# Kernel tuning notes

Hardware: AMD Instinct MI355X
Metric: run time of the kernel (lower is better)

## Reference

```python
import jax, jax.numpy as jnp
import numpy as np

EPS = 1e-5


def _rln(x, w, b, m1w, m1b, m2w, m2b):
    # Revised LayerNorm (DehazeFormer): per-sample stats over (C,H,W)
    mean = jnp.mean(x, axis=(1, 2, 3), keepdims=True)            # [b,1,1,1]
    std = jnp.sqrt(jnp.mean((x - mean) ** 2, axis=(1, 2, 3), keepdims=True) + EPS)
    normed = (x - mean) / std * w + b                            # [b,C,H,W]
    rescale = std * m1w + m1b                                    # 1x1 conv from 1 channel
    rebias = mean * m2w + m2b
    return normed, rescale, rebias


def _pconv(x, W, b):
    # 1x1 conv as channel contraction: W [out,in], x [b,in,h,w]
    return jnp.einsum('oi,bihw->bohw', W, x) + b[None, :, None, None]


def setup_inputs() -> dict:
    key = jax.random.key(0)
    ks = jax.random.split(key, 24)
    B, C, H, W = 8, 96, 128, 128
    p = lambda k, shp, s=0.02: (jax.random.normal(k, shp, dtype=jnp.float32) * s)
    inp = {
        'x_u': jax.random.normal(ks[0], (B, C, H, W), dtype=jnp.float32),
        'x_d': jax.random.normal(ks[1], (B, C, H, W), dtype=jnp.float32),
        # RLN (u)
        'nw_u': jnp.ones((1, C, 1, 1), jnp.float32),
        'nb_u': jnp.zeros((1, C, 1, 1), jnp.float32),
        'm1w_u': p(ks[2], (1, C, 1, 1)), 'm1b_u': p(ks[3], (1, C, 1, 1)),
        'm2w_u': p(ks[4], (1, C, 1, 1)), 'm2b_u': p(ks[5], (1, C, 1, 1)),
        # RLN (d)
        'nw_d': jnp.ones((1, C, 1, 1), jnp.float32),
        'nb_d': jnp.zeros((1, C, 1, 1), jnp.float32),
        'm1w_d': p(ks[6], (1, C, 1, 1)), 'm1b_d': p(ks[7], (1, C, 1, 1)),
        'm2w_d': p(ks[8], (1, C, 1, 1)), 'm2b_d': p(ks[9], (1, C, 1, 1)),
        # 1x1 qkv convs
        'Wqkv_u': p(ks[10], (2 * C, C)), 'bqkv_u': jnp.zeros((2 * C,), jnp.float32),
        'Wqkv_d': p(ks[11], (2 * C, C)), 'bqkv_d': jnp.zeros((2 * C,), jnp.float32),
        # learned scalar scales
        'scale_h': jnp.ones((1,), jnp.float32),
        'scale_w': jnp.ones((1,), jnp.float32),
        'scale_c': jnp.ones((1,), jnp.float32),
    }
    return inp


def reference(x_u, x_d,
              nw_u, nb_u, m1w_u, m1b_u, m2w_u, m2b_u,
              nw_d, nb_d, m1w_d, m1b_d, m2w_d, m2b_d,
              Wqkv_u, bqkv_u, Wqkv_d, bqkv_d,
              scale_h, scale_w, scale_c):
    x_d_norm, resc_d, bias_d = _rln(x_d, nw_d, nb_d, m1w_d, m1b_d, m2w_d, m2b_d)
    x_u_norm, resc_u, bias_u = _rln(x_u, nw_u, nb_u, m1w_u, m1b_u, m2w_u, m2b_u)

    q_u, v_u = jnp.split(_pconv(x_u_norm, Wqkv_u, bqkv_u), 2, axis=1)
    k_d, v_d = jnp.split(_pconv(x_d_norm, Wqkv_d, bqkv_d), 2, axis=1)

    q_h, q_w, q_c = jnp.split(q_u, 3, axis=1)
    k_h, k_w, k_c = jnp.split(k_d, 3, axis=1)
    vu_h, vu_w, vu_c = jnp.split(v_u, 3, axis=1)
    vd_h, vd_w, vd_c = jnp.split(v_d, 3, axis=1)

    # ---- height-axis attention: per (b,w), scores over h x h ----
    A_h = jax.nn.softmax(jnp.einsum('bciw,bcjw->bwij', q_h, k_h) * scale_h[0], axis=-1)
    d2u_h = jnp.einsum('bwij,bcjw->bciw', A_h, vd_h)            # attn @ v_d
    u2d_h = jnp.einsum('bwij,bciw->bcjw', A_h, vu_h)            # attn^T @ v_u

    # ---- width-axis attention: per (b,h), scores over w x w ----
    S_w = jnp.einsum('bchi,bchj->bhij', q_w, k_w) * scale_w[0]
    d2u_w = jnp.einsum('bhij,bchj->bchi', jax.nn.softmax(S_w, axis=-1), vd_w)
    # softmax(S_w^T, -1) @ v_u  ==  softmax over axis -2, contracted over i
    u2d_w = jnp.einsum('bhij,bchi->bchj', jax.nn.softmax(S_w, axis=-2), vu_w)

    # ---- channel-axis attention: per b, scores over c x c ----
    b, c, h, w = q_c.shape
    qc = q_c.reshape(b, c, h * w)
    kc = k_c.reshape(b, c, h * w)
    A_c = jax.nn.softmax(jnp.einsum('bcn,bdn->bcd', qc, kc) * scale_c[0], axis=-1)
    d2u_c = jnp.einsum('bcd,bdn->bcn', A_c, vd_c.reshape(b, c, h * w)).reshape(b, c, h, w)
    # NOTE: original code uses the same (non-transposed) softmax for u2d_c
    u2d_c = jnp.einsum('bcd,bdn->bcn', A_c, vu_c.reshape(b, c, h * w)).reshape(b, c, h, w)

    x_d2u = jnp.concatenate([d2u_h, d2u_w, d2u_c], axis=1)
    x_u2d = jnp.concatenate([u2d_h, u2d_w, u2d_c], axis=1)

    out_u = x_d2u * resc_u + bias_u + x_u
    out_d = x_u2d * resc_d + bias_d + x_d
    return out_u + out_d
```

## Files before the change

### kernel.cpp

```cpp
#include <hip/hip_runtime.h>
#include <math.h>

#define NB 8
#define NC 96
#define NH 128
#define NWID 128
#define NN (NH*NWID)
#define NCO 192
#define NM (NC*NN)

#define WS_SUMS   0
#define WS_SC     32
#define WS_AC     8224
#define WS_SU     16416
#define WS_TU     17184
#define WS_SD     17952
#define WS_TD     18720
#define WS_RU     19488
#define WS_RD     20256
#define WS_CADD   21024
#define WS_BPU    21792
#define WS_BPD    23328
#define WS_WB16   24864
#define WS_QKV16  327680
#define QKV16_D   25165824ull
#define WS_SLABS  25493504
#define OFF_QH    0ull
#define OFF_KH    5242880ull
#define OFF_QW    10485760ull
#define OFF_KW    15728640ull
#define OFF_VHU   20971520ull
#define OFF_VHD   25427968ull
#define OFF_VWU   29884416ull
#define OFF_VWD   34340864ull
#define WS_OH     44892160

typedef __attribute__((ext_vector_type(8))) short bf16x8;
typedef __attribute__((ext_vector_type(4))) float f32x4;

static __device__ __forceinline__ float bf2f(ushort u){ return __uint_as_float(((uint)u) << 16); }
static __device__ __forceinline__ ushort f2bf(float f){
  uint b = __float_as_uint(f);
  return (ushort)((b + 0x7fffu + ((b >> 16) & 1u)) >> 16);
}
static __device__ __forceinline__ bf16x8 ldfrag(const ushort* p){
  union { uint4 u; bf16x8 b; } cv; cv.u = *(const uint4*)p; return cv.b;
}

__global__ __launch_bounds__(256) void reduce_stats(const float* __restrict__ xu,
                                                    const float* __restrict__ xd,
                                                    float* __restrict__ ws) {
  int blk = blockIdx.x;
  int tensor = blk >> 9;
  int b = (blk >> 6) & 7;
  int chunk = blk & 63;
  const float* x = tensor ? xd : xu;
  const float4* p = (const float4*)(x + (size_t)b*NM + (size_t)chunk*(NM/64));
  float s = 0.f, sq = 0.f;
  for (int r = 0; r < 24; r++) {
    float4 v = p[threadIdx.x + r*256];
    s  += v.x + v.y + v.z + v.w;
    sq += v.x*v.x + v.y*v.y + v.z*v.z + v.w*v.w;
  }
  for (int o = 32; o; o >>= 1) { s += __shfl_down(s, o); sq += __shfl_down(sq, o); }
  __shared__ float ls[8];
  int wv = threadIdx.x >> 6, ln = threadIdx.x & 63;
  if (ln == 0) { ls[wv*2] = s; ls[wv*2+1] = sq; }
  __syncthreads();
  if (threadIdx.x == 0) {
    s  = ls[0] + ls[2] + ls[4] + ls[6];
    sq = ls[1] + ls[3] + ls[5] + ls[7];
    atomicAdd(&ws[WS_SUMS + (tensor*8 + b)*2],     s);
    atomicAdd(&ws[WS_SUMS + (tensor*8 + b)*2 + 1], sq);
  }
}

__global__ void compute_params(float* __restrict__ ws,
    const float* __restrict__ nwu, const float* __restrict__ nbu,
    const float* __restrict__ m1wu, const float* __restrict__ m1bu,
    const float* __restrict__ m2wu, const float* __restrict__ m2bu,
    const float* __restrict__ nwd, const float* __restrict__ nbd,
    const float* __restrict__ m1wd, const float* __restrict__ m1bd,
    const float* __restrict__ m2wd, const float* __restrict__ m2bd,
    const float* __restrict__ Wqu, const float* __restrict__ bqu,
    const float* __restrict__ Wqd, const float* __restrict__ bqd) {
  __shared__ float meanL[16], stdL[16];
  __shared__ float tuL[768], tdL[768];
  int t = threadIdx.x;
  if (t < 16) {
    float s = ws[WS_SUMS + t*2], sq = ws[WS_SUMS + t*2 + 1];
    const float inv = 1.f / (float)NM;
    float mean = s * inv;
    float var  = sq * inv - mean*mean;
    meanL[t] = mean;
    stdL[t]  = sqrtf(var + 1e-5f);
  }
  __syncthreads();
  for (int idx = t; idx < 768; idx += 256) {
    int b = idx / 96, c = idx % 96;
    float mu = meanL[b],   su = stdL[b];
    float md = meanL[8+b], sd = stdL[8+b];
    float scu = nwu[c] / su;
    float scd = nwd[c] / sd;
    float tcu = nbu[c] - mu*scu;
    float tcd = nbd[c] - md*scd;
    tuL[idx] = tcu; tdL[idx] = tcd;
    ws[WS_SU+idx] = scu; ws[WS_TU+idx] = tcu;
    ws[WS_SD+idx] = scd; ws[WS_TD+idx] = tcd;
    ws[WS_RU+idx] = su*m1wu[c] + m1bu[c];
    ws[WS_RD+idx] = sd*m1wd[c] + m1bd[c];
    ws[WS_CADD+idx] = (mu*m2wu[c] + m2bu[c]) + (md*m2wd[c] + m2bd[c]);
  }
  __syncthreads();
  for (int idx = t; idx < 3072; idx += 256) {
    int tensor = idx / 1536;
    int r = idx % 1536;
    int b = r / 192, o = r % 192;
    const float* Wq = tensor ? Wqd : Wqu;
    const float* tt = tensor ? tdL : tuL;
    float acc = tensor ? bqd[o] : bqu[o];
    for (int i = 0; i < 96; i++) acc += Wq[o*96 + i] * tt[b*96 + i];
    ws[(tensor ? WS_BPD : WS_BPU) + r] = acc;
  }
}

__global__ __launch_bounds__(256) void compute_wprime(float* __restrict__ ws,
    const float* __restrict__ Wqu, const float* __restrict__ Wqd) {
  int idx = blockIdx.x*256 + threadIdx.x;
  if (idx >= 319488) return;
  int tensor = idx / 159744;
  int r = idx % 159744;
  int b  = r / 19968;
  int r2 = r % 19968;
  int o  = r2 / 104, i = r2 % 104;
  ushort* wb = (ushort*)(ws + WS_WB16);
  ushort v = 0;
  if (i < 96) {
    const float* Wq = tensor ? Wqd : Wqu;
    const float* s  = ws + (tensor ? WS_SD : WS_SU);
    v = f2bf(Wq[o*96 + i] * s[b*96 + i]);
  }
  wb[idx] = v;
}

__global__ __launch_bounds__(256) void qkv_gemm(float* __restrict__ ws,
    const float* __restrict__ xu, const float* __restrict__ xd) {
  __shared__ __align__(16) ushort QL[33280];
  ushort* Al = QL;
  ushort* Bl = QL + 19968;
  int blk = blockIdx.x;
  int tensor = blk >> 10;
  int rem = blk & 1023;
  int b = rem >> 7;
  int nt = rem & 127;
  int n0 = nt*128;
  const float* x = (tensor ? xd : xu) + (size_t)b*NM;
  const ushort* wb = (const ushort*)(ws + WS_WB16) + (size_t)(tensor*8 + b)*19968;
  const float* bp = ws + (tensor ? WS_BPD : WS_BPU) + b*192;
  ushort* outq16 = (ushort*)(ws + WS_QKV16) + (tensor ? QKV16_D : 0) + (size_t)b*NCO*NN;
  ushort* slab = (ushort*)(ws + WS_SLABS);
  const int t = threadIdx.x;
  const int wv = t >> 6, lid = t & 63, l15 = lid & 15, l4 = lid >> 4;

  for (int it = 0; it < 10; it++) {
    int idx = t + it*256;
    if (idx < 2496) ((uint4*)Al)[idx] = ((const uint4*)wb)[idx];
  }
  for (int it = 0; it < 6; it++) {
    int idx = t + it*256;
    int i2 = (idx & 7) | ((idx >> 8) << 3);
    int n4 = (idx >> 3) & 31;
    const float* r0 = x + (size_t)(2*i2)*NN + n0 + n4*4;
    float4 a0 = *(const float4*)r0;
    float4 a1 = *(const float4*)(r0 + NN);
    uint p0 = (uint)f2bf(a0.x) | ((uint)f2bf(a1.x) << 16);
    uint p1 = (uint)f2bf(a0.y) | ((uint)f2bf(a1.y) << 16);
    uint p2 = (uint)f2bf(a0.z) | ((uint)f2bf(a1.z) << 16);
    uint p3 = (uint)f2bf(a0.w) | ((uint)f2bf(a1.w) << 16);
    ushort* base = &Bl[(size_t)(n4*4)*104 + 2*i2];
    *(uint*)(base)           = p0;
    *(uint*)(base + 104)     = p1;
    *(uint*)(base + 208)     = p2;
    *(uint*)(base + 312)     = p3;
  }
  __syncthreads();

  f32x4 z4 = {0.f,0.f,0.f,0.f};
  f32x4 acc[12][2];
  #pragma unroll
  for (int mt = 0; mt < 12; mt++) { acc[mt][0] = z4; acc[mt][1] = z4; }
  #pragma unroll
  for (int s = 0; s < 3; s++) {
    bf16x8 b0 = ldfrag(&Bl[((2*wv+0)*16 + l15)*104 + s*32 + l4*8]);
    bf16x8 b1 = ldfrag(&Bl[((2*wv+1)*16 + l15)*104 + s*32 + l4*8]);
    #pragma unroll
    for (int mt = 0; mt < 12; mt++) {
      bf16x8 a = ldfrag(&Al[(mt*16 + l15)*104 + s*32 + l4*8]);
      acc[mt][0] = __builtin_amdgcn_mfma_f32_16x16x32_bf16(a, b0, acc[mt][0], 0, 0, 0);
      acc[mt][1] = __builtin_amdgcn_mfma_f32_16x16x32_bf16(a, b1, acc[mt][1], 0, 0, 0);
    }
  }
  __syncthreads();
  ushort* Cl = QL;
  #pragma unroll
  for (int mt = 0; mt < 12; mt++) {
    #pragma unroll
    for (int r = 0; r < 4; r++) {
      int o = mt*16 + l4*4 + r;
      float bb = bp[o];
      Cl[o*128 + 32*wv + l15]      = f2bf(acc[mt][0][r] + bb);
      Cl[o*128 + 32*wv + 16 + l15] = f2bf(acc[mt][1][r] + bb);
    }
  }
  __syncthreads();
  for (int it = 0; it < 6; it++) {
    int idx = t + it*256;
    int lr = idx >> 4, ch = idx & 15;
    int o = (lr < 64) ? (64 + lr) : (96 + lr);
    *(uint4*)(outq16 + (size_t)o*NN + n0 + ch*8) = *(const uint4*)&Cl[o*128 + ch*8];
  }
  {
    int axis = t >> 7, w = t & 127;
    ushort* dstq = slab + (tensor ? (axis ? OFF_KW : OFF_KH) : (axis ? OFF_QW : OFF_QH));
    size_t o = axis ? ((size_t)(b*128 + nt)*128 + w)*40
                    : ((size_t)(b*128 + w)*128 + nt)*40;
    uint uu[16];
    #pragma unroll
    for (int k = 0; k < 16; k++) {
      ushort a0 = Cl[(axis*32 + 2*k)*128 + w];
      ushort a1 = Cl[(axis*32 + 2*k + 1)*128 + w];
      uu[k] = (uint)a0 | ((uint)a1 << 16);
    }
    *(uint4*)(dstq + o)      = make_uint4(uu[0],uu[1],uu[2],uu[3]);
    *(uint4*)(dstq + o + 8)  = make_uint4(uu[4],uu[5],uu[6],uu[7]);
    *(uint4*)(dstq + o + 16) = make_uint4(uu[8],uu[9],uu[10],uu[11]);
    *(uint4*)(dstq + o + 24) = make_uint4(uu[12],uu[13],uu[14],uu[15]);
  }
  {
    ushort* dstv = slab + (tensor ? OFF_VWD : OFF_VWU);
    for (int k = 0; k < 2; k++) {
      int idx = t + k*256;
      int c = idx >> 4, ch = idx & 15;
      *(uint4*)(dstv + ((size_t)(b*128 + nt)*32 + c)*136 + ch*8) =
          *(const uint4*)&Cl[(128 + c)*128 + ch*8];
    }
  }
}

__global__ __launch_bounds__(256) void qkv_prep(float* __restrict__ ws) {
  __shared__ __align__(16) ushort Br[16*1320];
  int bid = blockIdx.x;
  int tensor = bid >> 8;
  int r = bid & 255;
  int cb = r >> 7, b = (r >> 4) & 7, hb = (r >> 2) & 3, wb = r & 3;
  const ushort* qkv16 = (const ushort*)(ws + WS_QKV16);
  const ushort* src = qkv16 + (tensor ? QKV16_D : 0)
                    + (size_t)b*NCO*NN + (size_t)(96 + cb*16)*NN;
  ushort* dst = (ushort*)(ws + WS_SLABS) + (tensor ? OFF_VHD : OFF_VHU);
  int t = threadIdx.x;
  for (int k = 0; k < 8; k++) {
    int idx = t + k*256;
    int c = idx >> 7, h = (idx >> 2) & 31, w8 = idx & 3;
    uint4 v = *(const uint4*)(src + (size_t)c*NN + (size_t)(hb*32 + h)*NWID + wb*32 + w8*8);
    *(uint4*)&Br[c*1320 + h*40 + w8*8] = v;
  }
  __syncthreads();
  for (int k = 0; k < 2; k++) {
    int idx = t + k*256;
    int w = idx >> 4, c = idx & 15;
    uint uu[16];
    #pragma unroll
    for (int hh = 0; hh < 16; hh++) {
      ushort a0 = Br[c*1320 + (2*hh)*40 + w];
      ushort a1 = Br[c*1320 + (2*hh+1)*40 + w];
      uu[hh] = (uint)a0 | ((uint)a1 << 16);
    }
    size_t o = ((size_t)(b*128 + wb*32 + w)*32 + cb*16 + c)*136 + hb*32;
    *(uint4*)(dst + o)      = make_uint4(uu[0],uu[1],uu[2],uu[3]);
    *(uint4*)(dst + o + 8)  = make_uint4(uu[4],uu[5],uu[6],uu[7]);
    *(uint4*)(dst + o + 16) = make_uint4(uu[8],uu[9],uu[10],uu[11]);
    *(uint4*)(dst + o + 24) = make_uint4(uu[12],uu[13],uu[14],uu[15]);
  }
}

template<int AXIS>
__global__ __launch_bounds__(256) void attn_mfma(float* __restrict__ ws,
    const float* __restrict__ xu, const float* __restrict__ xd,
    float* __restrict__ out, const float* __restrict__ scale_p) {
  __shared__ __align__(16) ushort Qs[128*40];
  __shared__ __align__(16) ushort Ks[128*40];
  __shared__ __align__(16) ushort Vds[32*136];
  __shared__ __align__(16) ushort Vus[32*136];
  __shared__ __align__(16) ushort Pl[128*136];
  __shared__ float m1s[128], l1s[128];
  const int b = blockIdx.x >> 7, p2 = blockIdx.x & 127;
  const int t = threadIdx.x;
  const int wv = t >> 6, lid = t & 63, l15 = lid & 15, l4 = lid >> 4;
  const ushort* slab = (const ushort*)(ws + WS_SLABS);
  const ushort* qsrc  = slab + (AXIS ? OFF_QW : OFF_QH) + (size_t)(b*128 + p2)*5120;
  const ushort* ksrc  = slab + (AXIS ? OFF_KW : OFF_KH) + (size_t)(b*128 + p2)*5120;
  const ushort* vdsrc = slab + (AXIS ? OFF_VWD : OFF_VHD) + (size_t)(b*128 + p2)*4352;
  const ushort* vusrc = slab + (AXIS ? OFF_VWU : OFF_VHU) + (size_t)(b*128 + p2)*4352;
  for (int i = t; i < 2368; i += 256) {
    const uint4* s; uint4* d;
    if (i < 640)       { s = (const uint4*)qsrc + i;          d = (uint4*)Qs + i; }
    else if (i < 1280) { s = (const uint4*)ksrc + (i-640);    d = (uint4*)Ks + (i-640); }
    else if (i < 1824) { s = (const uint4*)vdsrc + (i-1280);  d = (uint4*)Vds + (i-1280); }
    else               { s = (const uint4*)vusrc + (i-1824);  d = (uint4*)Vus + (i-1824); }
    *d = *s;
  }
  const float sc = scale_p[0];
  const int cbas = AXIS ? 32 : 0;
  float ruv0 = ws[WS_RU + b*96 + cbas + l15];
  float ruv1 = ws[WS_RU + b*96 + cbas + 16 + l15];
  float rdv0 = ws[WS_RD + b*96 + cbas + l15];
  float rdv1 = ws[WS_RD + b*96 + cbas + 16 + l15];
  __syncthreads();

  f32x4 z4 = {0.f,0.f,0.f,0.f};
  f32x4 s1[2][8];
  {
    bf16x8 bfr[8];
    #pragma unroll
    for (int tj = 0; tj < 8; tj++) bfr[tj] = ldfrag(&Ks[(tj*16 + l15)*40 + l4*8]);
    #pragma unroll
    for (int ti = 0; ti < 2; ti++) {
      bf16x8 a = ldfrag(&Qs[((2*wv+ti)*16 + l15)*40 + l4*8]);
      #pragma unroll
      for (int tj = 0; tj < 8; tj++)
        s1[ti][tj] = __builtin_amdgcn_mfma_f32_16x16x32_bf16(a, bfr[tj], z4, 0, 0, 0);
    }
  }
  #pragma unroll
  for (int ti = 0; ti < 2; ti++) {
    #pragma unroll
    for (int r = 0; r < 4; r++) {
      float mx = -3.0e38f;
      #pragma unroll
      for (int tj = 0; tj < 8; tj++) { float v = s1[ti][tj][r]*sc; s1[ti][tj][r] = v; mx = fmaxf(mx, v); }
      mx = fmaxf(mx, __shfl_xor(mx, 1)); mx = fmaxf(mx, __shfl_xor(mx, 2));
      mx = fmaxf(mx, __shfl_xor(mx, 4)); mx = fmaxf(mx, __shfl_xor(mx, 8));
      float sm = 0.f;
      #pragma unroll
      for (int tj = 0; tj < 8; tj++) { float e = __expf(s1[ti][tj][r] - mx); s1[ti][tj][r] = e; sm += e; }
      sm += __shfl_xor(sm, 1); sm += __shfl_xor(sm, 2); sm += __shfl_xor(sm, 4); sm += __shfl_xor(sm, 8);
      int row = 32*wv + ti*16 + l4*4 + r;
      if (l15 == 0) { m1s[row] = mx; l1s[row] = sm; }
      float inv = __fdividef(1.f, sm);
      #pragma unroll
      for (int tj = 0; tj < 8; tj++) Pl[row*136 + tj*16 + l15] = f2bf(s1[ti][tj][r]*inv);
    }
  }
  __syncthreads();
  f32x4 o1[2][2] = {{z4,z4},{z4,z4}};
  #pragma unroll
  for (int ks = 0; ks < 4; ks++) {
    bf16x8 bv0 = ldfrag(&Vds[l15*136 + ks*32 + l4*8]);
    bf16x8 bv1 = ldfrag(&Vds[(16 + l15)*136 + ks*32 + l4*8]);
    #pragma unroll
    for (int mt = 0; mt < 2; mt++) {
      bf16x8 a = ldfrag(&Pl[((2*wv+mt)*16 + l15)*136 + ks*32 + l4*8]);
      o1[mt][0] = __builtin_amdgcn_mfma_f32_16x16x32_bf16(a, bv0, o1[mt][0], 0, 0, 0);
      o1[mt][1] = __builtin_amdgcn_mfma_f32_16x16x32_bf16(a, bv1, o1[mt][1], 0, 0, 0);
    }
  }
  {
    bf16x8 bq[8];
    #pragma unroll
    for (int it = 0; it < 8; it++) bq[it] = ldfrag(&Qs[(it*16 + l15)*40 + l4*8]);
    #pragma unroll
    for (int tjt = 0; tjt < 2; tjt++) {
      bf16x8 a = ldfrag(&Ks[((2*wv+tjt)*16 + l15)*40 + l4*8]);
      #pragma unroll
      for (int it = 0; it < 8; it++)
        s1[tjt][it] = __builtin_amdgcn_mfma_f32_16x16x32_bf16(a, bq[it], z4, 0, 0, 0);
    }
  }
  if (AXIS == 1) {
    #pragma unroll
    for (int tjt = 0; tjt < 2; tjt++) {
      #pragma unroll
      for (int r = 0; r < 4; r++) {
        float mx = -3.0e38f;
        #pragma unroll
        for (int it = 0; it < 8; it++) { float v = s1[tjt][it][r]*sc; s1[tjt][it][r] = v; mx = fmaxf(mx, v); }
        mx = fmaxf(mx, __shfl_xor(mx, 1)); mx = fmaxf(mx, __shfl_xor(mx, 2));
        mx = fmaxf(mx, __shfl_xor(mx, 4)); mx = fmaxf(mx, __shfl_xor(mx, 8));
        float sm = 0.f;
        #pragma unroll
        for (int it = 0; it < 8; it++) { float e = __expf(s1[tjt][it][r] - mx); s1[tjt][it][r] = e; sm += e; }
        sm += __shfl_xor(sm, 1); sm += __shfl_xor(sm, 2); sm += __shfl_xor(sm, 4); sm += __shfl_xor(sm, 8);
        float inv = __fdividef(1.f, sm);
        #pragma unroll
        for (int it = 0; it < 8; it++) s1[tjt][it][r] *= inv;
      }
    }
  } else {
    float mi[8], li[8];
    #pragma unroll
    for (int it = 0; it < 8; it++) {
      mi[it] = m1s[it*16 + l15];
      li[it] = __fdividef(1.f, l1s[it*16 + l15]);
    }
    #pragma unroll
    for (int tjt = 0; tjt < 2; tjt++)
      #pragma unroll
      for (int it = 0; it < 8; it++)
        #pragma unroll
        for (int r = 0; r < 4; r++)
          s1[tjt][it][r] = __expf(s1[tjt][it][r]*sc - mi[it]) * li[it];
  }
  __syncthreads();
  #pragma unroll
  for (int tjt = 0; tjt < 2; tjt++)
    #pragma unroll
    for (int r = 0; r < 4; r++) {
      int row = 32*wv + tjt*16 + l4*4 + r;
      #pragma unroll
      for (int it = 0; it < 8; it++) Pl[row*136 + it*16 + l15] = f2bf(s1[tjt][it][r]);
    }
  __syncthreads();
  f32x4 o2[2][2] = {{z4,z4},{z4,z4}};
  #pragma unroll
  for (int ks = 0; ks < 4; ks++) {
    bf16x8 bv0 = ldfrag(&Vus[l15*136 + ks*32 + l4*8]);
    bf16x8 bv1 = ldfrag(&Vus[(16 + l15)*136 + ks*32 + l4*8]);
    #pragma unroll
    for (int mt = 0; mt < 2; mt++) {
      bf16x8 a = ldfrag(&Pl[((2*wv+mt)*16 + l15)*136 + ks*32 + l4*8]);
      o2[mt][0] = __builtin_amdgcn_mfma_f32_16x16x32_bf16(a, bv0, o2[mt][0], 0, 0, 0);
      o2[mt][1] = __builtin_amdgcn_mfma_f32_16x16x32_bf16(a, bv1, o2[mt][1], 0, 0, 0);
    }
  }
  __syncthreads();
  float* St = (float*)Pl;
  #pragma unroll
  for (int mt = 0; mt < 2; mt++)
    #pragma unroll
    for (int nt = 0; nt < 2; nt++) {
      float ru = nt ? ruv1 : ruv0;
      float rd = nt ? rdv1 : rdv0;
      float4 vv;
      vv.x = o1[mt][nt][0]*ru + o2[mt][nt][0]*rd;
      vv.y = o1[mt][nt][1]*ru + o2[mt][nt][1]*rd;
      vv.z = o1[mt][nt][2]*ru + o2[mt][nt][2]*rd;
      vv.w = o1[mt][nt][3]*ru + o2[mt][nt][3]*rd;
      *(float4*)&St[(nt*16 + l15)*132 + (2*wv+mt)*16 + l4*4] = vv;
    }
  __syncthreads();
  if (AXIS == 1) {
    for (int k = 0; k < 4; k++) {
      int idx = t + k*256;
      int c = idx >> 5, p4 = idx & 31;
      float4 v = *(const float4*)&St[c*132 + p4*4];
      float ca = ws[WS_CADD + b*96 + 32 + c];
      size_t off = ((size_t)(b*NC + 32 + c)*NH + p2)*NWID + p4*4;
      float4 a = *(const float4*)(xu + off);
      float4 dd = *(const float4*)(xd + off);
      v.x += ca + a.x + dd.x; v.y += ca + a.y + dd.y;
      v.z += ca + a.z + dd.z; v.w += ca + a.w + dd.w;
      *(float4*)(out + off) = v;
    }
  } else {
    float* oh = ws + WS_OH;
    for (int k = 0; k < 4; k++) {
      int idx = t + k*256;
      int c = idx >> 5, p4 = idx & 31;
      float4 v = *(const float4*)&St[c*132 + p4*4];
      *(float4*)(oh + ((size_t)(b*128 + p2)*32 + c)*128 + p4*4) = v;
    }
  }
}

__global__ __launch_bounds__(256) void merge_h(float* __restrict__ ws,
    const float* __restrict__ xu, const float* __restrict__ xd,
    float* __restrict__ out) {
  __shared__ float T[32][33];
  int bid = blockIdx.x;
  int b = bid >> 9, c = (bid >> 4) & 31, ht = (bid >> 2) & 3, wt = bid & 3;
  int t = threadIdx.x;
  const float* oh = ws + WS_OH;
  {
    int w = t >> 3, h4 = t & 7;
    float4 v = *(const float4*)(oh + ((size_t)(b*128 + wt*32 + w)*32 + c)*128 + ht*32 + h4*4);
    T[w][h4*4+0] = v.x; T[w][h4*4+1] = v.y; T[w][h4*4+2] = v.z; T[w][h4*4+3] = v.w;
  }
  __syncthreads();
  {
    int h = t >> 3, w4 = t & 7;
    float ca = ws[WS_CADD + b*96 + c];
    size_t off = ((size_t)(b*NC + c)*NH + ht*32 + h)*NWID + wt*32 + w4*4;
    float4 a = *(const float4*)(xu + off);
    float4 d = *(const float4*)(xd + off);
    float4 v;
    v.x = T[w4*4+0][h] + ca + a.x + d.x;
    v.y = T[w4*4+1][h] + ca + a.y + d.y;
    v.z = T[w4*4+2][h] + ca + a.z + d.z;
    v.w = T[w4*4+3][h] + ca + a.w + d.w;
    *(float4*)(out + off) = v;
  }
}

__global__ __launch_bounds__(256) void attn_c1(float* __restrict__ ws) {
  __shared__ float qs[32][260], ks[32][260];
  int b = blockIdx.x >> 6, chunk = blockIdx.x & 63;
  int n0 = chunk * 256;
  int t = threadIdx.x;
  const ushort* qkv16 = (const ushort*)(ws + WS_QKV16);
  const ushort* qp = qkv16 + ((size_t)b*NCO + 64)*NN + n0;
  const ushort* kp = qkv16 + QKV16_D + ((size_t)b*NCO + 64)*NN + n0;
  for (int r = 0; r < 4; r++) {
    int idx = t + r*256;
    int c = idx >> 5, n8 = idx & 31;
    uint4 v = *(const uint4*)(qp + (size_t)c*NN + n8*8);
    uint4 w = *(const uint4*)(kp + (size_t)c*NN + n8*8);
    float* q = &qs[c][n8*8];
    float* kk = &ks[c][n8*8];
    q[0] = bf2f((ushort)(v.x & 0xffff)); q[1] = bf2f((ushort)(v.x >> 16));
    q[2] = bf2f((ushort)(v.y & 0xffff)); q[3] = bf2f((ushort)(v.y >> 16));
    q[4] = bf2f((ushort)(v.z & 0xffff)); q[5] = bf2f((ushort)(v.z >> 16));
    q[6] = bf2f((ushort)(v.w & 0xffff)); q[7] = bf2f((ushort)(v.w >> 16));
    kk[0] = bf2f((ushort)(w.x & 0xffff)); kk[1] = bf2f((ushort)(w.x >> 16));
    kk[2] = bf2f((ushort)(w.y & 0xffff)); kk[3] = bf2f((ushort)(w.y >> 16));
    kk[4] = bf2f((ushort)(w.z & 0xffff)); kk[5] = bf2f((ushort)(w.z >> 16));
    kk[6] = bf2f((ushort)(w.w & 0xffff)); kk[7] = bf2f((ushort)(w.w >> 16));
  }
  __syncthreads();
  int d = t & 31, cbq = t >> 5;
  float a[4] = {0.f,0.f,0.f,0.f};
  for (int n4 = 0; n4 < 64; n4++) {
    float4 kv = *(const float4*)&ks[d][n4*4];
    #pragma unroll
    for (int r = 0; r < 4; r++) {
      float4 qv = *(const float4*)&qs[cbq + 8*r][n4*4];
      a[r] += qv.x*kv.x + qv.y*kv.y + qv.z*kv.z + qv.w*kv.w;
    }
  }
  #pragma unroll
  for (int r = 0; r < 4; r++)
    atomicAdd(&ws[WS_SC + b*1024 + (cbq + 8*r)*32 + d], a[r]);
}

__global__ void attn_c2(float* __restrict__ ws, const float* __restrict__ scale_p) {
  int b = blockIdx.x, c = threadIdx.x;
  if (c >= 32) return;
  float sc = scale_p[0];
  float row[32];
  float m = -3.0e38f;
  for (int d = 0; d < 32; d++) { row[d] = ws[WS_SC + b*1024 + c*32 + d] * sc; m = fmaxf(m, row[d]); }
  float s = 0.f;
  for (int d = 0; d < 32; d++) { row[d] = __expf(row[d] - m); s += row[d]; }
  float inv = 1.f / s;
  for (int d = 0; d < 32; d++) ws[WS_AC + b*1024 + c*32 + d] = row[d]*inv;
}

__global__ __launch_bounds__(256) void attn_c3(float* __restrict__ ws,
    const float* __restrict__ xu, const float* __restrict__ xd,
    float* __restrict__ out) {
  __shared__ float AsT[32][36];
  __shared__ float ruL[32], rdL[32], caL[32];
  int b = blockIdx.x >> 6, chunk = blockIdx.x & 63;
  int t = threadIdx.x;
  for (int r = 0; r < 4; r++) {
    int idx = t + r*256;
    int c = idx >> 5, d = idx & 31;
    AsT[d][c] = ws[WS_AC + b*1024 + idx];
  }
  if (t < 32) {
    ruL[t] = ws[WS_RU + b*96 + 64 + t];
    rdL[t] = ws[WS_RD + b*96 + 64 + t];
    caL[t] = ws[WS_CADD + b*96 + 64 + t];
  }
  __syncthreads();
  int n = chunk*256 + t;
  const ushort* qkv16 = (const ushort*)(ws + WS_QKV16);
  const ushort* vdp = qkv16 + QKV16_D + ((size_t)b*NCO + 160)*NN + n;
  const ushort* vup = qkv16 + ((size_t)b*NCO + 160)*NN + n;
  float acc1[32], acc2[32];
  #pragma unroll
  for (int c2 = 0; c2 < 32; c2++) { acc1[c2]=0.f; acc2[c2]=0.f; }
  for (int d = 0; d < 32; d++) {
    float vd = bf2f(vdp[(size_t)d*NN]);
    float vu = bf2f(vup[(size_t)d*NN]);
    #pragma unroll
    for (int c4 = 0; c4 < 8; c4++) {
      float4 av = *(const float4*)&AsT[d][c4*4];
      acc1[c4*4+0] += av.x*vd; acc2[c4*4+0] += av.x*vu;
      acc1[c4*4+1] += av.y*vd; acc2[c4*4+1] += av.y*vu;
      acc1[c4*4+2] += av.z*vd; acc2[c4*4+2] += av.z*vu;
      acc1[c4*4+3] += av.w*vd; acc2[c4*4+3] += av.w*vu;
    }
  }
  size_t base = ((size_t)(b*NC) + 64)*NN + n;
  #pragma unroll
  for (int c2 = 0; c2 < 32; c2++) {
    size_t off = base + (size_t)c2*NN;
    out[off] = acc1[c2]*ruL[c2] + acc2[c2]*rdL[c2] + caL[c2] + xu[off] + xd[off];
  }
}

extern "C" void kernel_launch(void* const* d_in, const int* in_sizes, int n_in,
                              void* d_out, int out_size, void* d_ws, size_t ws_size,
                              hipStream_t stream) {
  (void)in_sizes; (void)n_in; (void)out_size; (void)ws_size;
  const float* xu   = (const float*)d_in[0];
  const float* xd   = (const float*)d_in[1];
  const float* nwu  = (const float*)d_in[2];
  const float* nbu  = (const float*)d_in[3];
  const float* m1wu = (const float*)d_in[4];
  const float* m1bu = (const float*)d_in[5];
  const float* m2wu = (const float*)d_in[6];
  const float* m2bu = (const float*)d_in[7];
  const float* nwd  = (const float*)d_in[8];
  const float* nbd  = (const float*)d_in[9];
  const float* m1wd = (const float*)d_in[10];
  const float* m1bd = (const float*)d_in[11];
  const float* m2wd = (const float*)d_in[12];
  const float* m2bd = (const float*)d_in[13];
  const float* Wqu  = (const float*)d_in[14];
  const float* bqu  = (const float*)d_in[15];
  const float* Wqd  = (const float*)d_in[16];
  const float* bqd  = (const float*)d_in[17];
  const float* sch  = (const float*)d_in[18];
  const float* scw  = (const float*)d_in[19];
  const float* scc  = (const float*)d_in[20];
  float* ws  = (float*)d_ws;
  float* out = (float*)d_out;

  hipMemsetAsync(d_ws, 0, 8224*sizeof(float), stream);
  reduce_stats<<<1024, 256, 0, stream>>>(xu, xd, ws);
  compute_params<<<1, 256, 0, stream>>>(ws, nwu, nbu, m1wu, m1bu, m2wu, m2bu,
                                        nwd, nbd, m1wd, m1bd, m2wd, m2bd,
                                        Wqu, bqu, Wqd, bqd);
  compute_wprime<<<1248, 256, 0, stream>>>(ws, Wqu, Wqd);
  qkv_gemm<<<2048, 256, 0, stream>>>(ws, xu, xd);
  qkv_prep<<<512, 256, 0, stream>>>(ws);
  attn_mfma<0><<<1024, 256, 0, stream>>>(ws, xu, xd, out, sch);
  attn_mfma<1><<<1024, 256, 0, stream>>>(ws, xu, xd, out, scw);
  merge_h<<<4096, 256, 0, stream>>>(ws, xu, xd, out);
  attn_c1<<<512, 256, 0, stream>>>(ws);
  attn_c2<<<8, 64, 0, stream>>>(ws, scc);
  attn_c3<<<512, 256, 0, stream>>>(ws, xu, xd, out);
}
```

Measured before the change: 256.7 us.

## Read QKV weights directly from global, pad output tile, store H-attention output as bf16

```diff
diff --git a/kernel.cpp b/kernel.cpp
--- a/kernel.cpp
+++ b/kernel.cpp
@@ -145,9 +145,8 @@
 
 __global__ __launch_bounds__(256) void qkv_gemm(float* __restrict__ ws,
     const float* __restrict__ xu, const float* __restrict__ xd) {
-  __shared__ __align__(16) ushort QL[33280];
-  ushort* Al = QL;
-  ushort* Bl = QL + 19968;
+  __shared__ __align__(16) ushort QL[26112];
+  ushort* Bl = QL;
   int blk = blockIdx.x;
   int tensor = blk >> 10;
   int rem = blk & 1023;
@@ -162,10 +161,6 @@
   const int t = threadIdx.x;
   const int wv = t >> 6, lid = t & 63, l15 = lid & 15, l4 = lid >> 4;
 
-  for (int it = 0; it < 10; it++) {
-    int idx = t + it*256;
-    if (idx < 2496) ((uint4*)Al)[idx] = ((const uint4*)wb)[idx];
-  }
   for (int it = 0; it < 6; it++) {
     int idx = t + it*256;
     int i2 = (idx & 7) | ((idx >> 8) << 3);
@@ -195,7 +190,7 @@
     bf16x8 b1 = ldfrag(&Bl[((2*wv+1)*16 + l15)*104 + s*32 + l4*8]);
     #pragma unroll
     for (int mt = 0; mt < 12; mt++) {
-      bf16x8 a = ldfrag(&Al[(mt*16 + l15)*104 + s*32 + l4*8]);
+      bf16x8 a = ldfrag(&wb[(mt*16 + l15)*104 + s*32 + l4*8]);
       acc[mt][0] = __builtin_amdgcn_mfma_f32_16x16x32_bf16(a, b0, acc[mt][0], 0, 0, 0);
       acc[mt][1] = __builtin_amdgcn_mfma_f32_16x16x32_bf16(a, b1, acc[mt][1], 0, 0, 0);
     }
@@ -208,8 +203,8 @@
     for (int r = 0; r < 4; r++) {
       int o = mt*16 + l4*4 + r;
       float bb = bp[o];
-      Cl[o*128 + 32*wv + l15]      = f2bf(acc[mt][0][r] + bb);
-      Cl[o*128 + 32*wv + 16 + l15] = f2bf(acc[mt][1][r] + bb);
+      Cl[o*136 + 32*wv + l15]      = f2bf(acc[mt][0][r] + bb);
+      Cl[o*136 + 32*wv + 16 + l15] = f2bf(acc[mt][1][r] + bb);
     }
   }
   __syncthreads();
@@ -217,7 +212,7 @@
     int idx = t + it*256;
     int lr = idx >> 4, ch = idx & 15;
     int o = (lr < 64) ? (64 + lr) : (96 + lr);
-    *(uint4*)(outq16 + (size_t)o*NN + n0 + ch*8) = *(const uint4*)&Cl[o*128 + ch*8];
+    *(uint4*)(outq16 + (size_t)o*NN + n0 + ch*8) = *(const uint4*)&Cl[o*136 + ch*8];
   }
   {
     int axis = t >> 7, w = t & 127;
@@ -227,8 +222,8 @@
     uint uu[16];
     #pragma unroll
     for (int k = 0; k < 16; k++) {
-      ushort a0 = Cl[(axis*32 + 2*k)*128 + w];
-      ushort a1 = Cl[(axis*32 + 2*k + 1)*128 + w];
+      ushort a0 = Cl[(axis*32 + 2*k)*136 + w];
+      ushort a1 = Cl[(axis*32 + 2*k + 1)*136 + w];
       uu[k] = (uint)a0 | ((uint)a1 << 16);
     }
     *(uint4*)(dstq + o)      = make_uint4(uu[0],uu[1],uu[2],uu[3]);
@@ -242,7 +237,7 @@
       int idx = t + k*256;
       int c = idx >> 4, ch = idx & 15;
       *(uint4*)(dstv + ((size_t)(b*128 + nt)*32 + c)*136 + ch*8) =
-          *(const uint4*)&Cl[(128 + c)*128 + ch*8];
+          *(const uint4*)&Cl[(128 + c)*136 + ch*8];
     }
   }
 }
@@ -462,12 +457,17 @@
       *(float4*)(out + off) = v;
     }
   } else {
-    float* oh = ws + WS_OH;
-    for (int k = 0; k < 4; k++) {
+    ushort* oh16 = (ushort*)(ws + WS_OH);
+    for (int k = 0; k < 2; k++) {
       int idx = t + k*256;
-      int c = idx >> 5, p4 = idx & 31;
-      float4 v = *(const float4*)&St[c*132 + p4*4];
-      *(float4*)(oh + ((size_t)(b*128 + p2)*32 + c)*128 + p4*4) = v;
+      int c = idx >> 4, p8 = idx & 15;
+      const float* src = &St[c*132 + p8*8];
+      uint4 pk;
+      pk.x = (uint)f2bf(src[0]) | ((uint)f2bf(src[1]) << 16);
+      pk.y = (uint)f2bf(src[2]) | ((uint)f2bf(src[3]) << 16);
+      pk.z = (uint)f2bf(src[4]) | ((uint)f2bf(src[5]) << 16);
+      pk.w = (uint)f2bf(src[6]) | ((uint)f2bf(src[7]) << 16);
+      *(uint4*)(oh16 + ((size_t)(b*128 + p2)*32 + c)*128 + p8*8) = pk;
     }
   }
 }
@@ -479,11 +479,14 @@
   int bid = blockIdx.x;
   int b = bid >> 9, c = (bid >> 4) & 31, ht = (bid >> 2) & 3, wt = bid & 3;
   int t = threadIdx.x;
-  const float* oh = ws + WS_OH;
+  const ushort* oh16 = (const ushort*)(ws + WS_OH);
   {
-    int w = t >> 3, h4 = t & 7;
-    float4 v = *(const float4*)(oh + ((size_t)(b*128 + wt*32 + w)*32 + c)*128 + ht*32 + h4*4);
-    T[w][h4*4+0] = v.x; T[w][h4*4+1] = v.y; T[w][h4*4+2] = v.z; T[w][h4*4+3] = v.w;
+    int w = t >> 3, hq = t & 7;
+    uint2 v = *(const uint2*)(oh16 + ((size_t)(b*128 + wt*32 + w)*32 + c)*128 + ht*32 + hq*4);
+    T[w][hq*4+0] = bf2f((ushort)(v.x & 0xffff));
+    T[w][hq*4+1] = bf2f((ushort)(v.x >> 16));
+    T[w][hq*4+2] = bf2f((ushort)(v.y & 0xffff));
+    T[w][hq*4+3] = bf2f((ushort)(v.y >> 16));
   }
   __syncthreads();
   {
```

Measured after the change: 284.1 us. 10.7% more time.
